# Kernel optimization log

Measured on AMD Instinct MI355X. Metric: run time of the kernel, lower is better.

The kernel has to match this reference:

```python
import jax, jax.numpy as jnp
import numpy as np

T, D, H, B = 2048, 1152, 16, 8
DH = D // H  # 72


def _apply_rope(x, cos_h, sin_h):
    # x: [T, H, DH]; cos_h, sin_h: [T, DH//2] (already chunked halves)
    c = jnp.concatenate([cos_h, cos_h], axis=-1)[:, None, :]  # [T,1,DH]
    s = jnp.concatenate([sin_h, sin_h], axis=-1)[:, None, :]
    x1, x2 = jnp.split(x, 2, axis=-1)
    rot = jnp.concatenate([-x2, x1], axis=-1)
    return x * c + rot * s


def setup_inputs() -> dict:
    key = jax.random.key(0)
    ks = jax.random.split(key, 12)
    hidden_states = jax.random.normal(ks[0], (T, D), jnp.float32)
    inner = jnp.sort(jax.random.randint(ks[1], (B - 1,), 1, T))
    cu_seqlens = jnp.concatenate(
        [jnp.zeros((1,), jnp.int32), inner.astype(jnp.int32), jnp.full((1,), T, jnp.int32)])
    cos = jax.random.uniform(ks[2], (T, DH), jnp.float32, -1.0, 1.0)
    sin = jax.random.uniform(ks[3], (T, DH), jnp.float32, -1.0, 1.0)
    std = 0.02
    Wq = jax.random.normal(ks[4], (D, D), jnp.float32) * std
    Wk = jax.random.normal(ks[5], (D, D), jnp.float32) * std
    Wv = jax.random.normal(ks[6], (D, D), jnp.float32) * std
    Wo = jax.random.normal(ks[7], (D, D), jnp.float32) * std
    bq = jnp.zeros((D,), jnp.float32)
    bk = jnp.zeros((D,), jnp.float32)
    bv = jnp.zeros((D,), jnp.float32)
    bo = jnp.zeros((D,), jnp.float32)
    return {"hidden_states": hidden_states, "cu_seqlens": cu_seqlens,
            "cos": cos, "sin": sin,
            "Wq": Wq, "bq": bq, "Wk": Wk, "bk": bk,
            "Wv": Wv, "bv": bv, "Wo": Wo, "bo": bo}


def reference(hidden_states, cu_seqlens, cos, sin, Wq, bq, Wk, bk, Wv, bv, Wo, bo):
    t = hidden_states.shape[0]
    scale = DH ** -0.5
    q = (hidden_states @ Wq.T + bq).reshape(t, H, DH)
    k = (hidden_states @ Wk.T + bk).reshape(t, H, DH)
    v = (hidden_states @ Wv.T + bv).reshape(t, H, DH)
    # RoPE: cos/sin [T, DH] are chunked in half along last dim, first half used
    cos_h = cos[:, : DH // 2]
    sin_h = sin[:, : DH // 2]
    q = _apply_rope(q, cos_h, sin_h)
    k = _apply_rope(k, cos_h, sin_h)
    # segment ids from cu_seqlens -> block-diagonal (varlen) attention mask
    pos = jnp.arange(t)
    seg = jnp.searchsorted(cu_seqlens, pos, side='right') - 1  # [T]
    mask = seg[:, None] == seg[None, :]  # [T, T]
    scores = jnp.einsum('thd,shd->hts', q, k) * scale  # [H, T, T]
    scores = jnp.where(mask[None], scores, jnp.float32(-1e30))
    attn = jax.nn.softmax(scores, axis=-1)
    out = jnp.einsum('hts,shd->thd', attn, v).reshape(t, D)
    return out @ Wo.T + bo
```

## Files before the change

### kernel.cpp

```cpp
#include <hip/hip_runtime.h>

#define TT 2048
#define DM 1152
#define NHEAD 16
#define HDIM 72
#define HDP 96
#define HDV 80
#define KSPLIT 2

typedef __attribute__((ext_vector_type(8))) __bf16 bf16x8;
typedef __attribute__((ext_vector_type(4))) float f32x4;
typedef unsigned short u16;
typedef unsigned int u32;
typedef __attribute__((ext_vector_type(4))) u16 u16x4;

__device__ inline u16 f2bf(float f){
  u32 u = __builtin_bit_cast(u32, f);
  return (u16)((u + 0x7FFFu + ((u >> 16) & 1u)) >> 16);
}
__device__ inline float bf2f(u16 v){
  return __builtin_bit_cast(float, ((u32)v) << 16);
}
__device__ inline bf16x8 ldb8(const u16* p){
  uint4 u = *(const uint4*)p;
  return __builtin_bit_cast(bf16x8, u);
}
__device__ inline f32x4 mfma16(bf16x8 a, bf16x8 b, f32x4 c){
  return __builtin_amdgcn_mfma_f32_16x16x32_bf16(a, b, c, 0, 0, 0);
}
__device__ inline void gload_lds16(const u16* g, u16* l){
  __builtin_amdgcn_global_load_lds(
      (const __attribute__((address_space(1))) void*)g,
      (__attribute__((address_space(3))) void*)l, 16, 0, 0);
}

__global__ void k_convert(const float* hid, const float* wq, const float* wk,
                          const float* wv, const float* wo, const int* cu,
                          u16* hb, u16* wqb, u16* wkb, u16* wvb, u16* wob,
                          u16* qhb, u16* khb, int* seg)
{
  long i = (long)blockIdx.x * blockDim.x + threadIdx.x;
  const long NHID4 = (long)TT * DM / 4;
  const long NW4 = (long)DM * DM / 4;
  const long NC4 = NHID4 + 4*NW4;
  if (i < NC4) {
    const float4* src; u16* dst; long o;
    if (i < NHID4) { src = (const float4*)hid; dst = hb; o = i; }
    else {
      long j = i - NHID4;
      int w = (int)(j / NW4);
      o = j - (long)w * NW4;
      src = (const float4*)((w==0)?wq:(w==1)?wk:(w==2)?wv:wo);
      dst = (w==0)?wqb:(w==1)?wkb:(w==2)?wvb:wob;
    }
    float4 v = src[o];
    u16x4 r; r.x = f2bf(v.x); r.y = f2bf(v.y); r.z = f2bf(v.z); r.w = f2bf(v.w);
    *(u16x4*)(dst + o*4) = r;
  } else {
    long j = i - NC4;
    const long PER = (long)NHEAD*TT*12;
    if (j < 2*PER) {
      int arr = (int)(j / PER);
      long r = j - (long)arr*PER;
      long th = r / 12;
      int c = (int)(r - th*12);
      ((u32*)(arr ? khb : qhb))[th*48 + 36 + c] = 0u;
    }
  }
  if (i < TT) {
    int c = 0;
    for (int e = 0; e < 9; ++e) c += (cu[e] <= (int)i);
    seg[i] = c - 1;
  }
}

__device__ __forceinline__ void gemm_m128n64(const u16* __restrict__ A,
                                             const u16* __restrict__ W,
                                             const float* __restrict__ bias,
                                             void* out, int mode, float oscale)
{
  __shared__ __align__(16) u16 As[2][128*32];
  __shared__ __align__(16) u16 Bs[2][64*32];
  int tid = threadIdx.x;
  int lane = tid & 63, wid = tid >> 6;
  int l15 = lane & 15, quad = lane >> 4;
  int bm = blockIdx.x * 128, bn = blockIdx.y * 64;
  int wm = wid*32;
  f32x4 acc[2][4] = {};
  const u16* ga = A + (long)(bm + (tid>>2))*DM + (tid&3)*8;
  const u16* gb = W + (long)(bn + (tid>>2))*DM + (tid&3)*8;
  {
    u16* lA = As[0] + wid*512; u16* lB = Bs[0] + wid*512;
    gload_lds16(ga,          lA);
    gload_lds16(ga + 64*DM,  lA + 2048);
    gload_lds16(gb,          lB);
  }
  int cur = 0;
  for (int k0 = 0; k0 < DM; k0 += 32, cur ^= 1) {
    __syncthreads();
    if (k0 + 32 < DM) {
      u16* lA = As[cur^1] + wid*512; u16* lB = Bs[cur^1] + wid*512;
      gload_lds16(ga + k0 + 32,          lA);
      gload_lds16(ga + k0 + 32 + 64*DM,  lA + 2048);
      gload_lds16(gb + k0 + 32,          lB);
    }
    bf16x8 af[2], bfr[4];
    for (int i=0;i<2;i++) af[i]  = ldb8(As[cur] + (wm + i*16 + l15)*32 + quad*8);
    for (int i=0;i<4;i++) bfr[i] = ldb8(Bs[cur] + (i*16 + l15)*32 + quad*8);
    for (int mi=0;mi<2;mi++)
      for (int ni=0;ni<4;ni++)
        acc[mi][ni] = mfma16(af[mi], bfr[ni], acc[mi][ni]);
  }
  for (int ni=0;ni<4;ni++){
    int n = bn + ni*16 + l15;
    float bv_ = bias[n];
    int h = n / HDIM, dh = n - (n / HDIM)*HDIM;
    for (int mi=0;mi<2;mi++){
      int m0 = bm + wm + mi*16 + quad*4;
      for (int r=0;r<4;r++){
        float v = (acc[mi][ni][r] + bv_) * oscale;
        int m = m0 + r;
        if (mode == 0) {
          ((u16*)out)[((long)(h*TT + m))*HDP + dh] = f2bf(v);
        } else {
          ((u16*)out)[((long)(h*HDV + dh))*TT + m] = f2bf(v);
        }
      }
    }
  }
}

__global__ __launch_bounds__(256, 4) void k_gemm_qkv(const u16* __restrict__ A,
    const u16* __restrict__ Wq, const u16* __restrict__ Wk, const u16* __restrict__ Wv,
    const float* __restrict__ bq, const float* __restrict__ bk, const float* __restrict__ bv,
    u16* oq, u16* ok, u16* ov)
{
  const float scale = 0.11785113019775793f;
  int z = blockIdx.z;
  if (z == 0)      gemm_m128n64(A, Wq, bq, oq, 0, scale);
  else if (z == 1) gemm_m128n64(A, Wk, bk, ok, 0, 1.0f);
  else             gemm_m128n64(A, Wv, bv, ov, 2, 1.0f);
}

__global__ __launch_bounds__(256, 4) void k_gemm_o(const u16* __restrict__ A,
    const u16* __restrict__ W, const float* __restrict__ bias, float* out)
{
  __shared__ __align__(16) u16 As[2][64*32];
  __shared__ __align__(16) u16 Bs[2][64*32];
  int tid = threadIdx.x;
  int lane = tid & 63, wid = tid >> 6;
  int l15 = lane & 15, quad = lane >> 4;
  int bm = blockIdx.x * 64, bn = blockIdx.y * 64;
  int wm = (wid>>1)*32, wn = (wid&1)*32;
  f32x4 acc[2][2] = {};
  const u16* ga = A + (long)(bm + (tid>>2))*DM + (tid&3)*8;
  const u16* gb = W + (long)(bn + (tid>>2))*DM + (tid&3)*8;
  {
    gload_lds16(ga, As[0] + wid*512);
    gload_lds16(gb, Bs[0] + wid*512);
  }
  int cur = 0;
  for (int k0 = 0; k0 < DM; k0 += 32, cur ^= 1) {
    __syncthreads();
    if (k0 + 32 < DM) {
      gload_lds16(ga + k0 + 32, As[cur^1] + wid*512);
      gload_lds16(gb + k0 + 32, Bs[cur^1] + wid*512);
    }
    bf16x8 af[2], bfr[2];
    for (int i=0;i<2;i++) af[i]  = ldb8(As[cur] + (wm + i*16 + l15)*32 + quad*8);
    for (int i=0;i<2;i++) bfr[i] = ldb8(Bs[cur] + (wn + i*16 + l15)*32 + quad*8);
    for (int mi=0;mi<2;mi++)
      for (int ni=0;ni<2;ni++)
        acc[mi][ni] = mfma16(af[mi], bfr[ni], acc[mi][ni]);
  }
  for (int ni=0;ni<2;ni++){
    int n = bn + wn + ni*16 + l15;
    float bv_ = bias[n];
    for (int mi=0;mi<2;mi++){
      int m0 = bm + wm + mi*16 + quad*4;
      for (int r=0;r<4;r++)
        out[(long)(m0 + r)*DM + n] = acc[mi][ni][r] + bv_;
    }
  }
}

__global__ void k_rope(u16* qh, u16* kh, const float* __restrict__ cosb,
                       const float* __restrict__ sinb)
{
  int i = blockIdx.x * blockDim.x + threadIdx.x;
  const int total = 2 * NHEAD * TT * 36;
  if (i >= total) return;
  int d = i % 36; int rest = i / 36;
  int t = rest % TT; rest /= TT;
  int h = rest % NHEAD; int qk = rest / NHEAD;
  u16* base = (qk ? kh : qh) + ((long)h*TT + t)*HDP;
  float x1 = bf2f(base[d]), x2 = bf2f(base[d+36]);
  float c = cosb[t*HDIM + d], s = sinb[t*HDIM + d];
  base[d]    = f2bf(x1*c - x2*s);
  base[d+36] = f2bf(x2*c + x1*s);
}

__global__ __launch_bounds__(256, 2) void k_attn(const u16* __restrict__ qh,
                                                 const u16* __restrict__ kh,
                                                 const u16* __restrict__ vT,
                                                 const int* __restrict__ seg,
                                                 const int* __restrict__ cu,
                                                 float* __restrict__ pacc,
                                                 float* __restrict__ plsum)
{
  __shared__ __align__(16) u16 Ks[2][64*96];
  __shared__ __align__(16) u16 pbuf[4][16][144];
  int h = blockIdx.y;
  int z = blockIdx.z;
  int tid = threadIdx.x, lane = tid & 63, wid = tid >> 6;
  int l15 = lane & 15, quad = lane >> 4;
  int qb0 = blockIdx.x * 128;
  int qbase = qb0 + wid*32;

  bf16x8 qf[2][3];
  int lo[2][4], hi[2][4];
  for (int t=0;t<2;t++){
    const u16* qp = qh + ((long)h*TT + qbase + t*16 + l15)*HDP + quad*8;
    qf[t][0] = ldb8(qp); qf[t][1] = ldb8(qp+32); qf[t][2] = ldb8(qp+64);
    for (int r=0;r<4;r++){
      int sq = seg[qbase + t*16 + quad*4 + r];
      lo[t][r] = cu[sq]; hi[t][r] = cu[sq+1];
    }
  }
  f32x4 acc[2][5] = {};
  float lsum[2][4] = {};

  int s_begin = cu[seg[qb0]] & ~63;
  int s_end = cu[seg[qb0 + 127] + 1];
  int nt = (s_end - s_begin + 63) >> 6;
  int nt0 = (nt + 1) >> 1;
  int it_lo = z ? nt0 : 0;
  int it_hi = z ? nt : nt0;

  const u16* kbase = kh + (long)h*TT*HDP;
  const u16* vbase = vT + ((long)h*HDV + l15)*TT + quad*8;

  if (it_lo < it_hi) {
    {
      const u16* gk = kbase + (long)(s_begin + it_lo*64)*HDP + tid*8;
      u16* lK = Ks[0] + wid*512;
      gload_lds16(gk,        lK);
      gload_lds16(gk + 2048, lK + 2048);
      gload_lds16(gk + 4096, lK + 4096);
    }
    for (int it = it_lo; it < it_hi; ++it) {
      int s0 = s_begin + it*64;
      int cur = (it - it_lo) & 1;
      __syncthreads();
      if (it + 1 < it_hi) {
        const u16* gk = kbase + (long)(s0 + 64)*HDP + tid*8;
        u16* lK = Ks[cur^1] + wid*512;
        gload_lds16(gk,        lK);
        gload_lds16(gk + 2048, lK + 2048);
        gload_lds16(gk + 4096, lK + 4096);
      }
      f32x4 sc[2][4] = {};
      for (int j=0;j<4;j++){
        const u16* kp = Ks[cur] + (j*16 + l15)*96 + quad*8;
        bf16x8 k0 = ldb8(kp), k1 = ldb8(kp+32), k2 = ldb8(kp+64);
        sc[0][j] = mfma16(qf[0][0], k0, sc[0][j]);
        sc[1][j] = mfma16(qf[1][0], k0, sc[1][j]);
        sc[0][j] = mfma16(qf[0][1], k1, sc[0][j]);
        sc[1][j] = mfma16(qf[1][1], k1, sc[1][j]);
        sc[0][j] = mfma16(qf[0][2], k2, sc[0][j]);
        sc[1][j] = mfma16(qf[1][2], k2, sc[1][j]);
      }
      for (int t=0;t<2;t++){
        for (int j=0;j<4;j++){
          int kidx = s0 + j*16 + l15;
          for (int r=0;r<4;r++){
            bool in = (kidx >= lo[t][r]) && (kidx < hi[t][r]);
            float p = in ? __expf(sc[t][j][r]) : 0.f;
            lsum[t][r] += p;
            pbuf[wid][quad*4+r][t*72 + j*16 + l15] = f2bf(p);
          }
        }
      }
      bf16x8 pf[2][2];
      for (int t=0;t<2;t++){
        pf[t][0] = ldb8(&pbuf[wid][l15][t*72 + quad*8]);
        pf[t][1] = ldb8(&pbuf[wid][l15][t*72 + 32 + quad*8]);
      }
      const u16* vp = vbase + s0;
      for (int n=0;n<5;n++){
        bf16x8 vf0 = ldb8(vp + (long)n*16*TT);
        bf16x8 vf1 = ldb8(vp + (long)n*16*TT + 32);
        acc[0][n] = mfma16(pf[0][0], vf0, acc[0][n]);
        acc[1][n] = mfma16(pf[1][0], vf0, acc[1][n]);
        acc[0][n] = mfma16(pf[0][1], vf1, acc[0][n]);
        acc[1][n] = mfma16(pf[1][1], vf1, acc[1][n]);
      }
    }
  }
  for (int off=1; off<16; off<<=1)
    for (int t=0;t<2;t++)
      for (int r=0;r<4;r++)
        lsum[t][r] += __shfl_xor(lsum[t][r], off, 64);
  for (int t=0;t<2;t++){
    for (int n=0;n<5;n++){
      int dh = n*16 + l15;
      for (int r=0;r<4;r++){
        int tk = qbase + t*16 + quad*4 + r;
        pacc[(((long)z*TT + tk)*NHEAD + h)*HDV + dh] = acc[t][n][r];
      }
    }
    if (l15 == 0){
      for (int r=0;r<4;r++){
        int tk = qbase + t*16 + quad*4 + r;
        plsum[((long)z*TT + tk)*NHEAD + h] = lsum[t][r];
      }
    }
  }
}

__global__ void k_combine(const float* __restrict__ pacc,
                          const float* __restrict__ plsum,
                          u16* __restrict__ ao)
{
  int i = blockIdx.x*blockDim.x + threadIdx.x;
  const int total = TT*NHEAD*HDIM;
  if (i >= total) return;
  int dh = i % HDIM; int rest = i / HDIM;
  int h = rest % NHEAD; int t = rest / NHEAD;
  long i0 = ((long)t*NHEAD + h)*HDV + dh;
  float a = pacc[i0] + pacc[(long)TT*NHEAD*HDV + i0];
  float l = plsum[t*NHEAD + h] + plsum[TT*NHEAD + t*NHEAD + h];
  ao[(long)t*DM + h*HDIM + dh] = f2bf(a / l);
}

extern "C" void kernel_launch(void* const* d_in, const int* in_sizes, int n_in,
                              void* d_out, int out_size, void* d_ws, size_t ws_size,
                              hipStream_t stream)
{
  const float* hid  = (const float*)d_in[0];
  const int*   cu   = (const int*)d_in[1];
  const float* cosb = (const float*)d_in[2];
  const float* sinb = (const float*)d_in[3];
  const float* wq   = (const float*)d_in[4];
  const float* bq   = (const float*)d_in[5];
  const float* wk   = (const float*)d_in[6];
  const float* bk   = (const float*)d_in[7];
  const float* wv   = (const float*)d_in[8];
  const float* bv   = (const float*)d_in[9];
  const float* wo   = (const float*)d_in[10];
  const float* bo   = (const float*)d_in[11];

  char* ws = (char*)d_ws;
  u16* hb  = (u16*)ws; ws += (long)TT*DM*2;
  u16* wqb = (u16*)ws; ws += (long)DM*DM*2;
  u16* wkb = (u16*)ws; ws += (long)DM*DM*2;
  u16* wvb = (u16*)ws; ws += (long)DM*DM*2;
  u16* wob = (u16*)ws; ws += (long)DM*DM*2;
  u16* qhb = (u16*)ws; ws += (long)NHEAD*TT*HDP*2;
  u16* khb = (u16*)ws; ws += (long)NHEAD*TT*HDP*2;
  u16* vTb = (u16*)ws; ws += (long)NHEAD*HDV*TT*2;
  u16* aob = (u16*)ws; ws += (long)TT*DM*2;
  int* seg = (int*)ws; ws += (long)TT*4;
  float* pacc  = (float*)ws; ws += (long)KSPLIT*TT*NHEAD*HDV*4;
  float* plsum = (float*)ws; ws += (long)KSPLIT*TT*NHEAD*4;

  long nconv = ((long)TT*DM + 4L*DM*DM)/4 + 2L*NHEAD*TT*12;
  k_convert<<<dim3((nconv + 255)/256), 256, 0, stream>>>(
      hid, wq, wk, wv, wo, cu, hb, wqb, wkb, wvb, wob, qhb, khb, seg);

  dim3 gqkv(TT/128, DM/64, 3);
  k_gemm_qkv<<<gqkv, 256, 0, stream>>>(hb, wqb, wkb, wvb, bq, bk, bv, qhb, khb, vTb);

  int nrope = 2*NHEAD*TT*36;
  k_rope<<<dim3((nrope + 255)/256), 256, 0, stream>>>(qhb, khb, cosb, sinb);

  dim3 ga(TT/128, NHEAD, KSPLIT);
  k_attn<<<ga, 256, 0, stream>>>(qhb, khb, vTb, seg, cu, pacc, plsum);

  int ncomb = TT*NHEAD*HDIM;
  k_combine<<<dim3((ncomb + 255)/256), 256, 0, stream>>>(pacc, plsum, aob);

  dim3 go(TT/64, DM/64);
  k_gemm_o<<<go, 256, 0, stream>>>(aob, wob, bo, (float*)d_out);
}
```

Measured before the change: 198.7 us.

## Load K tiles directly into registers with register prefetch instead of LDS

```diff
diff --git a/kernel.cpp b/kernel.cpp
--- a/kernel.cpp
+++ b/kernel.cpp
@@ -208,7 +208,6 @@
                                                  float* __restrict__ pacc,
                                                  float* __restrict__ plsum)
 {
-  __shared__ __align__(16) u16 Ks[2][64*96];
   __shared__ __align__(16) u16 pbuf[4][16][144];
   int h = blockIdx.y;
   int z = blockIdx.z;
@@ -241,34 +240,35 @@
   const u16* vbase = vT + ((long)h*HDV + l15)*TT + quad*8;
 
   if (it_lo < it_hi) {
+    bf16x8 kf[4][3];
     {
-      const u16* gk = kbase + (long)(s_begin + it_lo*64)*HDP + tid*8;
-      u16* lK = Ks[0] + wid*512;
-      gload_lds16(gk,        lK);
-      gload_lds16(gk + 2048, lK + 2048);
-      gload_lds16(gk + 4096, lK + 4096);
+      const u16* kp = kbase + (long)(s_begin + it_lo*64 + l15)*HDP + quad*8;
+      for (int j=0;j<4;j++)
+        for (int c=0;c<3;c++)
+          kf[j][c] = ldb8(kp + j*16*HDP + c*32);
     }
     for (int it = it_lo; it < it_hi; ++it) {
       int s0 = s_begin + it*64;
-      int cur = (it - it_lo) & 1;
-      __syncthreads();
-      if (it + 1 < it_hi) {
-        const u16* gk = kbase + (long)(s0 + 64)*HDP + tid*8;
-        u16* lK = Ks[cur^1] + wid*512;
-        gload_lds16(gk,        lK);
-        gload_lds16(gk + 2048, lK + 2048);
-        gload_lds16(gk + 4096, lK + 4096);
-      }
       f32x4 sc[2][4] = {};
       for (int j=0;j<4;j++){
-        const u16* kp = Ks[cur] + (j*16 + l15)*96 + quad*8;
-        bf16x8 k0 = ldb8(kp), k1 = ldb8(kp+32), k2 = ldb8(kp+64);
-        sc[0][j] = mfma16(qf[0][0], k0, sc[0][j]);
-        sc[1][j] = mfma16(qf[1][0], k0, sc[1][j]);
-        sc[0][j] = mfma16(qf[0][1], k1, sc[0][j]);
-        sc[1][j] = mfma16(qf[1][1], k1, sc[1][j]);
-        sc[0][j] = mfma16(qf[0][2], k2, sc[0][j]);
-        sc[1][j] = mfma16(qf[1][2], k2, sc[1][j]);
+        sc[0][j] = mfma16(qf[0][0], kf[j][0], sc[0][j]);
+        sc[1][j] = mfma16(qf[1][0], kf[j][0], sc[1][j]);
+        sc[0][j] = mfma16(qf[0][1], kf[j][1], sc[0][j]);
+        sc[1][j] = mfma16(qf[1][1], kf[j][1], sc[1][j]);
+        sc[0][j] = mfma16(qf[0][2], kf[j][2], sc[0][j]);
+        sc[1][j] = mfma16(qf[1][2], kf[j][2], sc[1][j]);
+      }
+      const u16* vp = vbase + s0;
+      bf16x8 vf[5][2];
+      for (int n=0;n<5;n++){
+        vf[n][0] = ldb8(vp + (long)n*16*TT);
+        vf[n][1] = ldb8(vp + (long)n*16*TT + 32);
+      }
+      if (it + 1 < it_hi) {
+        const u16* kp = kbase + (long)(s0 + 64 + l15)*HDP + quad*8;
+        for (int j=0;j<4;j++)
+          for (int c=0;c<3;c++)
+            kf[j][c] = ldb8(kp + j*16*HDP + c*32);
       }
       for (int t=0;t<2;t++){
         for (int j=0;j<4;j++){
@@ -286,14 +286,11 @@
         pf[t][0] = ldb8(&pbuf[wid][l15][t*72 + quad*8]);
         pf[t][1] = ldb8(&pbuf[wid][l15][t*72 + 32 + quad*8]);
       }
-      const u16* vp = vbase + s0;
       for (int n=0;n<5;n++){
-        bf16x8 vf0 = ldb8(vp + (long)n*16*TT);
-        bf16x8 vf1 = ldb8(vp + (long)n*16*TT + 32);
-        acc[0][n] = mfma16(pf[0][0], vf0, acc[0][n]);
-        acc[1][n] = mfma16(pf[1][0], vf0, acc[1][n]);
-        acc[0][n] = mfma16(pf[0][1], vf1, acc[0][n]);
-        acc[1][n] = mfma16(pf[1][1], vf1, acc[1][n]);
+        acc[0][n] = mfma16(pf[0][0], vf[n][0], acc[0][n]);
+        acc[1][n] = mfma16(pf[1][0], vf[n][0], acc[1][n]);
+        acc[0][n] = mfma16(pf[0][1], vf[n][1], acc[0][n]);
+        acc[1][n] = mfma16(pf[1][1], vf[n][1], acc[1][n]);
       }
     }
   }
```

Result: no change. 195.3 us (-1.7%).
